# Kernel optimization log

Hardware: AMD Instinct MI355X
Metric: run time of the kernel (lower is better)

## Reference

```python
import jax, jax.numpy as jnp
import numpy as np

B, T, N, D, H = 16, 12, 325, 64, 4
E = 2600
NEG_SLOPE = 0.2
LN_EPS = 1e-5
SM_EPS = 1e-16


def setup_inputs() -> dict:
    key = jax.random.key(0)
    ks = jax.random.split(key, 8)
    x = jax.random.normal(ks[0], (B, T, N, D), dtype=jnp.float32)
    edge_index = jax.random.randint(ks[1], (2, E), 0, N, dtype=jnp.int64)
    W = jax.random.normal(ks[2], (D, H, D), dtype=jnp.float32) * 0.05   # lin weight, [in, heads, out]
    att_src = jax.random.normal(ks[3], (H, D), dtype=jnp.float32) * 0.05
    att_dst = jax.random.normal(ks[4], (H, D), dtype=jnp.float32) * 0.05
    bias = jnp.zeros((D,), dtype=jnp.float32)
    gamma = jnp.ones((D,), dtype=jnp.float32)
    beta = jnp.zeros((D,), dtype=jnp.float32)
    return {"x": x, "W": W, "att_src": att_src, "att_dst": att_dst,
            "bias": bias, "gamma": gamma, "beta": beta, "edge_index": edge_index}


def reference(x, W, att_src, att_dst, bias, gamma, beta, edge_index):
    b, t, n, d = x.shape
    bt = b * t
    xb = x.reshape(bt, n, d)

    # add self-loops (GATConv default add_self_loops=True)
    loops = jnp.arange(n, dtype=edge_index.dtype)
    src = jnp.concatenate([edge_index[0], loops])  # message source j
    dst = jnp.concatenate([edge_index[1], loops])  # message target i

    # per-head linear projection, node axis leading for segment ops: [N, BT, H, D]
    xp = jnp.einsum('bnd,dhf->nbhf', xb, W)

    a_src = jnp.einsum('nbhf,hf->nbh', xp, att_src)  # [N, BT, H]
    a_dst = jnp.einsum('nbhf,hf->nbh', xp, att_dst)

    alpha = a_src[src] + a_dst[dst]                  # [Etot, BT, H]
    alpha = jnp.where(alpha >= 0, alpha, NEG_SLOPE * alpha)

    # segment softmax over incoming edges of each dst node
    m = jax.ops.segment_max(alpha, dst, num_segments=n)        # [N, BT, H]
    e = jnp.exp(alpha - m[dst])
    s = jax.ops.segment_sum(e, dst, num_segments=n)            # [N, BT, H]
    coef = e / (s[dst] + SM_EPS)                               # [Etot, BT, H]

    # weighted scatter-sum aggregation
    msgs = coef[..., None] * xp[src]                           # [Etot, BT, H, D]
    out = jax.ops.segment_sum(msgs, dst, num_segments=n)       # [N, BT, H, D]

    out = out.mean(axis=2) + bias                              # concat=False -> head mean; [N, BT, D]
    out = out.transpose(1, 0, 2).reshape(b, t, n, d)

    # residual + LayerNorm
    y = x + out
    mu = y.mean(axis=-1, keepdims=True)
    var = y.var(axis=-1, keepdims=True)
    return (y - mu) * jax.lax.rsqrt(var + LN_EPS) * gamma + beta
```

## Files before the change

### kernel.cpp

```cpp
#include <hip/hip_runtime.h>

#define Nn 325
#define Dd 64
#define Hh 4
#define Ee 2600
#define BT 192
#define ETOT (Ee+Nn)
#define NROWS (BT*Nn)
#define MAXDEG 48

typedef __attribute__((ext_vector_type(8))) short bf16x8;
typedef __attribute__((ext_vector_type(4))) float f32x4;

static __device__ __forceinline__ short f2bf(float f) {
    union { float f; unsigned u; } v; v.f = f;
    unsigned r = v.u + 0x7fffu + ((v.u >> 16) & 1u);
    return (short)(r >> 16);
}
static __device__ __forceinline__ float bf_lo(unsigned p) {
    union { unsigned u; float f; } v; v.u = p << 16; return v.f;
}
static __device__ __forceinline__ float bf_hi(unsigned p) {
    union { unsigned u; float f; } v; v.u = p & 0xffff0000u; return v.f;
}

__global__ __launch_bounds__(256) void k_pre(
    const float* __restrict__ W, unsigned short* __restrict__ Wt,
    const int* __restrict__ ei, int* __restrict__ offs, int* __restrict__ elist)
{
    const int t = threadIdx.x;
    if (blockIdx.x < 64) {
        const int f = blockIdx.x * 256 + t;
        const int thr = f >> 6, idx = f & 63;
        const int tl = idx >> 4, kk = (idx >> 3) & 1, j = idx & 7;
        const int w = thr >> 6, lane = thr & 63;
        const int q = lane >> 4, l16 = lane & 15;
        Wt[f] = (unsigned short)f2bf(
            W[(size_t)(kk * 32 + q * 8 + j) * 256 + w * 64 + tl * 16 + l16]);
        return;
    }
    __shared__ int cnt[Nn + 1];
    __shared__ int cur[Nn];
    const int lane = t & 63;
    for (int i = t; i <= Nn; i += 256) cnt[i] = 0;
    __syncthreads();
    for (int e = t; e < ETOT; e += 256) {
        int d = (e < Ee) ? ei[Ee + e] : (e - Ee);
        atomicAdd(&cnt[d + 1], 1);
    }
    __syncthreads();
    if (t < 64) {
        int run = 0;
        for (int c = 0; c < 6; ++c) {
            int i = c * 64 + lane;
            int v = (i <= Nn) ? cnt[i] : 0;
            #pragma unroll
            for (int off = 1; off < 64; off <<= 1) {
                int u = __shfl_up(v, off);
                if (lane >= off) v += u;
            }
            v += run;
            if (i <= Nn) cnt[i] = v;
            run = __shfl(v, 63);
        }
    }
    __syncthreads();
    for (int i = t; i <= Nn; i += 256) offs[i] = cnt[i];
    for (int i = t; i < Nn; i += 256) cur[i] = cnt[i];
    __syncthreads();
    for (int e = t; e < ETOT; e += 256) {
        int s, d;
        if (e < Ee) { s = ei[e]; d = ei[Ee + e]; }
        else        { s = e - Ee; d = e - Ee; }
        int slot = atomicAdd(&cur[d], 1);
        elist[slot] = s;
    }
}

__global__ __launch_bounds__(256) void k_proj(
    const float* __restrict__ x, const unsigned short* __restrict__ Wt,
    const float* __restrict__ att_src, const float* __restrict__ att_dst,
    unsigned short* __restrict__ xp, float* __restrict__ asrc,
    float* __restrict__ adst)
{
    const int t = threadIdx.x;
    const int w = t >> 6;
    const int lane = t & 63;
    const int q = lane >> 4;
    const int l16 = lane & 15;
    const int g0 = blockIdx.x * 32;

    bf16x8 bfr[4][2];
    const bf16x8* wtp = (const bf16x8*)(Wt + (size_t)t * 64);
    #pragma unroll
    for (int tl = 0; tl < 4; ++tl)
        #pragma unroll
        for (int kk = 0; kk < 2; ++kk)
            bfr[tl][kk] = wtp[tl * 2 + kk];

    bf16x8 afr[2][2];
    #pragma unroll
    for (int rt = 0; rt < 2; ++rt)
        #pragma unroll
        for (int kk = 0; kk < 2; ++kk) {
            const float* xr = x + (size_t)(g0 + rt * 16 + l16) * Dd + kk * 32 + q * 8;
            float4 a0 = *(const float4*)xr;
            float4 a1 = *(const float4*)(xr + 4);
            afr[rt][kk][0]=f2bf(a0.x); afr[rt][kk][1]=f2bf(a0.y);
            afr[rt][kk][2]=f2bf(a0.z); afr[rt][kk][3]=f2bf(a0.w);
            afr[rt][kk][4]=f2bf(a1.x); afr[rt][kk][5]=f2bf(a1.y);
            afr[rt][kk][6]=f2bf(a1.z); afr[rt][kk][7]=f2bf(a1.w);
        }

    f32x4 acc[2][4];
    #pragma unroll
    for (int rt = 0; rt < 2; ++rt)
        #pragma unroll
        for (int tl = 0; tl < 4; ++tl) {
            acc[rt][tl] = (f32x4){0.f, 0.f, 0.f, 0.f};
            acc[rt][tl] = __builtin_amdgcn_mfma_f32_16x16x32_bf16(afr[rt][0], bfr[tl][0], acc[rt][tl], 0, 0, 0);
            acc[rt][tl] = __builtin_amdgcn_mfma_f32_16x16x32_bf16(afr[rt][1], bfr[tl][1], acc[rt][tl], 0, 0, 0);
        }

    float avs[4], avd[4];
    #pragma unroll
    for (int tl = 0; tl < 4; ++tl) {
        avs[tl] = att_src[w * 64 + tl * 16 + l16];
        avd[tl] = att_dst[w * 64 + tl * 16 + l16];
    }
    #pragma unroll
    for (int rt = 0; rt < 2; ++rt)
        #pragma unroll
        for (int r = 0; r < 4; ++r) {
            float ps = 0.f, pd = 0.f;
            #pragma unroll
            for (int tl = 0; tl < 4; ++tl) {
                ps = fmaf(acc[rt][tl][r], avs[tl], ps);
                pd = fmaf(acc[rt][tl][r], avd[tl], pd);
            }
            #pragma unroll
            for (int off = 1; off < 16; off <<= 1) {
                ps += __shfl_xor(ps, off);
                pd += __shfl_xor(pd, off);
            }
            if (l16 == 0) {
                asrc[(size_t)(g0 + rt * 16 + q * 4 + r) * Hh + w] = ps;
                adst[(size_t)(g0 + rt * 16 + q * 4 + r) * Hh + w] = pd;
            }
        }

    __shared__ unsigned short ldsXP[32][264];
    #pragma unroll
    for (int rt = 0; rt < 2; ++rt)
        #pragma unroll
        for (int tl = 0; tl < 4; ++tl)
            #pragma unroll
            for (int r = 0; r < 4; ++r)
                ldsXP[rt * 16 + q * 4 + r][(tl * 16 + l16) * 4 + w] =
                    (unsigned short)f2bf(acc[rt][tl][r]);
    __syncthreads();
    #pragma unroll
    for (int c = 0; c < 4; ++c) {
        int idx = c * 256 + t;
        int row = idx >> 5;
        int off = (idx & 31) * 8;
        uint4 v = *(const uint4*)&ldsXP[row][off];
        *(uint4*)(xp + (size_t)(g0 + row) * 256 + off) = v;
    }
}

__global__ __launch_bounds__(512) void k_aggr(
    const unsigned short* __restrict__ xp, const float* __restrict__ asrc,
    const float* __restrict__ adst, const int* __restrict__ offs,
    const int* __restrict__ elist, const float* __restrict__ x,
    const float* __restrict__ bias, const float* __restrict__ gamma,
    const float* __restrict__ beta, float* __restrict__ out)
{
    const int wv   = threadIdx.x >> 6;
    const int lane = threadIdx.x & 63;
    const int xcd  = blockIdx.x & 7;
    const int wid  = (blockIdx.x >> 3) * 8 + wv;
    if (wid >= 12 * Nn) return;
    const int btp  = wid / Nn;
    const int n    = wid - btp * Nn;
    const int half = lane >> 5;
    const int bt   = (xcd * 12 + btp) * 2 + half;
    const int btN  = bt * Nn;
    const int row_i = btN + n;
    const int o0 = offs[n];
    int deg = offs[n + 1] - o0;
    if (deg > MAXDEG) deg = MAXDEG;
    const int el = (lane >> 2) & 7;
    const int h  = lane & 3;

    __shared__ float coefS[8][2][MAXDEG][4];
    __shared__ int   jS[8][MAXDEG];

    const float adi = adst[(size_t)row_i * Hh + h];

    float areg[6];
    #pragma unroll
    for (int it = 0; it < 6; ++it) {
        const int e = it * 8 + el;
        float a = -3e38f;
        if (e < deg) {
            const int j = elist[o0 + e];
            if (half == 0 && h == 0) jS[wv][e] = j;
            a = asrc[(size_t)(btN + j) * Hh + h] + adi;
        }
        areg[it] = (a >= 0.f) ? a : 0.2f * a;
    }
    float m = areg[0];
    #pragma unroll
    for (int it = 1; it < 6; ++it) m = fmaxf(m, areg[it]);
    #pragma unroll
    for (int off = 4; off <= 16; off <<= 1) m = fmaxf(m, __shfl_xor(m, off));
    float s = 0.f;
    #pragma unroll
    for (int it = 0; it < 6; ++it) { areg[it] = __expf(areg[it] - m); s += areg[it]; }
    #pragma unroll
    for (int off = 4; off <= 16; off <<= 1) s += __shfl_xor(s, off);
    const float inv_s = 1.f / (s + 1e-16f);
    #pragma unroll
    for (int it = 0; it < 6; ++it) {
        const int e = it * 8 + el;
        if (e < deg) coefS[wv][half][e][h] = areg[it] * inv_s;
    }

    const int fl = lane & 31;
    const int f0 = fl * 2;
    const unsigned short* xpbt = xp + (size_t)btN * 256 + fl * 8;
    float a0=0,a1=0,a2=0,a3=0,a4=0,a5=0,a6=0,a7=0;
    int e2 = 0;
    for (; e2 + 2 <= deg; e2 += 2) {
        const int jb0 = jS[wv][e2];
        const int jb1 = jS[wv][e2 + 1];
        const float4 c0 = *(const float4*)coefS[wv][half][e2];
        const float4 c1 = *(const float4*)coefS[wv][half][e2 + 1];
        const uint4 r0 = *(const uint4*)(xpbt + (size_t)jb0 * 256);
        const uint4 r1 = *(const uint4*)(xpbt + (size_t)jb1 * 256);
        a0 = fmaf(c0.x, bf_lo(r0.x), a0); a1 = fmaf(c0.y, bf_hi(r0.x), a1);
        a2 = fmaf(c0.z, bf_lo(r0.y), a2); a3 = fmaf(c0.w, bf_hi(r0.y), a3);
        a4 = fmaf(c0.x, bf_lo(r0.z), a4); a5 = fmaf(c0.y, bf_hi(r0.z), a5);
        a6 = fmaf(c0.z, bf_lo(r0.w), a6); a7 = fmaf(c0.w, bf_hi(r0.w), a7);
        a0 = fmaf(c1.x, bf_lo(r1.x), a0); a1 = fmaf(c1.y, bf_hi(r1.x), a1);
        a2 = fmaf(c1.z, bf_lo(r1.y), a2); a3 = fmaf(c1.w, bf_hi(r1.y), a3);
        a4 = fmaf(c1.x, bf_lo(r1.z), a4); a5 = fmaf(c1.y, bf_hi(r1.z), a5);
        a6 = fmaf(c1.z, bf_lo(r1.w), a6); a7 = fmaf(c1.w, bf_hi(r1.w), a7);
    }
    if (e2 < deg) {
        const int jb0 = jS[wv][e2];
        const float4 c0 = *(const float4*)coefS[wv][half][e2];
        const uint4 r0 = *(const uint4*)(xpbt + (size_t)jb0 * 256);
        a0 = fmaf(c0.x, bf_lo(r0.x), a0); a1 = fmaf(c0.y, bf_hi(r0.x), a1);
        a2 = fmaf(c0.z, bf_lo(r0.y), a2); a3 = fmaf(c0.w, bf_hi(r0.y), a3);
        a4 = fmaf(c0.x, bf_lo(r0.z), a4); a5 = fmaf(c0.y, bf_hi(r0.z), a5);
        a6 = fmaf(c0.z, bf_lo(r0.w), a6); a7 = fmaf(c0.w, bf_hi(r0.w), a7);
    }

    float2 bi = *(const float2*)(bias + f0);
    float2 xv = *(const float2*)(x + (size_t)row_i * Dd + f0);
    float y0 = xv.x + (a0 + a1 + a2 + a3) * 0.25f + bi.x;
    float y1 = xv.y + (a4 + a5 + a6 + a7) * 0.25f + bi.y;
    float s1 = y0 + y1, s2v = y0 * y0 + y1 * y1;
    #pragma unroll
    for (int off = 1; off <= 16; off <<= 1) {
        s1  += __shfl_xor(s1, off);
        s2v += __shfl_xor(s2v, off);
    }
    float mu  = s1 * (1.f / Dd);
    float var = s2v * (1.f / Dd) - mu * mu;
    float r = rsqrtf(var + 1e-5f);
    float2 ga = *(const float2*)(gamma + f0);
    float2 be = *(const float2*)(beta + f0);
    float2 o;
    o.x = (y0 - mu) * r * ga.x + be.x;
    o.y = (y1 - mu) * r * ga.y + be.y;
    *(float2*)(out + (size_t)row_i * Dd + f0) = o;
}

extern "C" void kernel_launch(void* const* d_in, const int* in_sizes, int n_in,
                              void* d_out, int out_size, void* d_ws, size_t ws_size,
                              hipStream_t stream)
{
    const float* x       = (const float*)d_in[0];
    const float* W       = (const float*)d_in[1];
    const float* att_src = (const float*)d_in[2];
    const float* att_dst = (const float*)d_in[3];
    const float* bias    = (const float*)d_in[4];
    const float* gamma   = (const float*)d_in[5];
    const float* beta    = (const float*)d_in[6];
    const int*   ei      = (const int*)d_in[7];

    unsigned short* xp = (unsigned short*)d_ws;
    unsigned short* Wt = xp + (size_t)NROWS * 256;
    float* asrc  = (float*)(Wt + 16384);
    float* adst  = asrc + (size_t)NROWS * Hh;
    int*   offs  = (int*)(adst + (size_t)NROWS * Hh);
    int*   elist = offs + (Nn + 1);
    float* out   = (float*)d_out;

    hipLaunchKernelGGL(k_pre, dim3(65), dim3(256), 0, stream, W, Wt, ei, offs, elist);
    hipLaunchKernelGGL(k_proj, dim3(NROWS / 32), dim3(256), 0, stream,
                       x, Wt, att_src, att_dst, xp, asrc, adst);
    hipLaunchKernelGGL(k_aggr, dim3(8 * 488), dim3(512), 0, stream,
                       xp, asrc, adst, offs, elist, x, bias, gamma, beta, out);
}
```

Baseline: 138.7 us.

## Pre-convert x to bf16 in prep kernel, prescale edge indices, trim softmax loops

The prep kernel gets 488 extra blocks that convert x to bf16 into a workspace buffer, so the projection kernel loads bf16 fragments directly instead of converting fp32. Edge source indices are stored pre-multiplied by 16 so the aggregation kernel can use byte-offset addressing. The softmax loops now stop early based on node degree. The residual and LayerNorm parameter loads are hoisted ahead of the gather loop. The extra bf16 pass adds a full read and write of x, which may cost more than the conversion it removes from the projection kernel.

```diff
diff --git a/kernel.cpp b/kernel.cpp
--- a/kernel.cpp
+++ b/kernel.cpp
@@ -26,7 +26,8 @@
 
 __global__ __launch_bounds__(256) void k_pre(
     const float* __restrict__ W, unsigned short* __restrict__ Wt,
-    const int* __restrict__ ei, int* __restrict__ offs, int* __restrict__ elist)
+    const int* __restrict__ ei, int* __restrict__ offs, int* __restrict__ elist,
+    const float* __restrict__ x, unsigned short* __restrict__ xbf)
 {
     const int t = threadIdx.x;
     if (blockIdx.x < 64) {
@@ -39,6 +40,23 @@
             W[(size_t)(kk * 32 + q * 8 + j) * 256 + w * 64 + tl * 16 + l16]);
         return;
     }
+    if (blockIdx.x >= 65) {
+        const int bx = blockIdx.x - 65;
+        #pragma unroll
+        for (int k = 0; k < 8; ++k) {
+            const int idx = bx * 2048 + k * 256 + t;
+            if (idx < (NROWS * Dd) / 4) {
+                float4 v = ((const float4*)x)[idx];
+                ushort4 o;
+                o.x = (unsigned short)f2bf(v.x);
+                o.y = (unsigned short)f2bf(v.y);
+                o.z = (unsigned short)f2bf(v.z);
+                o.w = (unsigned short)f2bf(v.w);
+                ((ushort4*)xbf)[idx] = o;
+            }
+        }
+        return;
+    }
     __shared__ int cnt[Nn + 1];
     __shared__ int cur[Nn];
     const int lane = t & 63;
@@ -73,12 +91,12 @@
         if (e < Ee) { s = ei[e]; d = ei[Ee + e]; }
         else        { s = e - Ee; d = e - Ee; }
         int slot = atomicAdd(&cur[d], 1);
-        elist[slot] = s;
+        elist[slot] = s * 16;
     }
 }
 
 __global__ __launch_bounds__(256) void k_proj(
-    const float* __restrict__ x, const unsigned short* __restrict__ Wt,
+    const unsigned short* __restrict__ xbf, const unsigned short* __restrict__ Wt,
     const float* __restrict__ att_src, const float* __restrict__ att_dst,
     unsigned short* __restrict__ xp, float* __restrict__ asrc,
     float* __restrict__ adst)
@@ -102,15 +120,9 @@
     #pragma unroll
     for (int rt = 0; rt < 2; ++rt)
         #pragma unroll
-        for (int kk = 0; kk < 2; ++kk) {
-            const float* xr = x + (size_t)(g0 + rt * 16 + l16) * Dd + kk * 32 + q * 8;
-            float4 a0 = *(const float4*)xr;
-            float4 a1 = *(const float4*)(xr + 4);
-            afr[rt][kk][0]=f2bf(a0.x); afr[rt][kk][1]=f2bf(a0.y);
-            afr[rt][kk][2]=f2bf(a0.z); afr[rt][kk][3]=f2bf(a0.w);
-            afr[rt][kk][4]=f2bf(a1.x); afr[rt][kk][5]=f2bf(a1.y);
-            afr[rt][kk][6]=f2bf(a1.z); afr[rt][kk][7]=f2bf(a1.w);
-        }
+        for (int kk = 0; kk < 2; ++kk)
+            afr[rt][kk] = *(const bf16x8*)(
+                xbf + (size_t)(g0 + rt * 16 + l16) * Dd + kk * 32 + q * 8);
 
     f32x4 acc[2][4];
     #pragma unroll
@@ -186,50 +198,65 @@
     const int half = lane >> 5;
     const int bt   = (xcd * 12 + btp) * 2 + half;
     const int btN  = bt * Nn;
+    const int btN16 = btN * 16;
     const int row_i = btN + n;
     const int o0 = offs[n];
     int deg = offs[n + 1] - o0;
     if (deg > MAXDEG) deg = MAXDEG;
+    const int nit = (deg + 7) >> 3;
     const int el = (lane >> 2) & 7;
     const int h  = lane & 3;
+    const int h4 = h * 4;
 
     __shared__ float coefS[8][2][MAXDEG][4];
     __shared__ int   jS[8][MAXDEG];
 
     const float adi = adst[(size_t)row_i * Hh + h];
+    const char* asrc_c = (const char*)asrc;
 
     float areg[6];
+    float m = -3e38f;
     #pragma unroll
     for (int it = 0; it < 6; ++it) {
+        if (it >= nit) break;
         const int e = it * 8 + el;
         float a = -3e38f;
         if (e < deg) {
-            const int j = elist[o0 + e];
-            if (half == 0 && h == 0) jS[wv][e] = j;
-            a = asrc[(size_t)(btN + j) * Hh + h] + adi;
-        }
-        areg[it] = (a >= 0.f) ? a : 0.2f * a;
-    }
-    float m = areg[0];
-    #pragma unroll
-    for (int it = 1; it < 6; ++it) m = fmaxf(m, areg[it]);
+            const int j16 = elist[o0 + e];
+            if (half == 0 && h == 0) jS[wv][e] = j16;
+            a = *(const float*)(asrc_c + (size_t)(unsigned)(btN16 + j16) + h4) + adi;
+        }
+        a = (a >= 0.f) ? a : 0.2f * a;
+        areg[it] = a;
+        m = fmaxf(m, a);
+    }
     #pragma unroll
     for (int off = 4; off <= 16; off <<= 1) m = fmaxf(m, __shfl_xor(m, off));
     float s = 0.f;
     #pragma unroll
-    for (int it = 0; it < 6; ++it) { areg[it] = __expf(areg[it] - m); s += areg[it]; }
+    for (int it = 0; it < 6; ++it) {
+        if (it >= nit) break;
+        areg[it] = __expf(areg[it] - m);
+        s += areg[it];
+    }
     #pragma unroll
     for (int off = 4; off <= 16; off <<= 1) s += __shfl_xor(s, off);
     const float inv_s = 1.f / (s + 1e-16f);
     #pragma unroll
     for (int it = 0; it < 6; ++it) {
+        if (it >= nit) break;
         const int e = it * 8 + el;
         if (e < deg) coefS[wv][half][e][h] = areg[it] * inv_s;
     }
 
     const int fl = lane & 31;
     const int f0 = fl * 2;
-    const unsigned short* xpbt = xp + (size_t)btN * 256 + fl * 8;
+    const float2 bi = *(const float2*)(bias + f0);
+    const float2 xv = *(const float2*)(x + (size_t)row_i * Dd + f0);
+    const float2 ga = *(const float2*)(gamma + f0);
+    const float2 be = *(const float2*)(beta + f0);
+
+    const char* xpb = (const char*)xp + (size_t)btN16 * 32 + fl * 16;
     float a0=0,a1=0,a2=0,a3=0,a4=0,a5=0,a6=0,a7=0;
     int e2 = 0;
     for (; e2 + 2 <= deg; e2 += 2) {
@@ -237,8 +264,8 @@
         const int jb1 = jS[wv][e2 + 1];
         const float4 c0 = *(const float4*)coefS[wv][half][e2];
         const float4 c1 = *(const float4*)coefS[wv][half][e2 + 1];
-        const uint4 r0 = *(const uint4*)(xpbt + (size_t)jb0 * 256);
-        const uint4 r1 = *(const uint4*)(xpbt + (size_t)jb1 * 256);
+        const uint4 r0 = *(const uint4*)(xpb + (size_t)(unsigned)jb0 * 32);
+        const uint4 r1 = *(const uint4*)(xpb + (size_t)(unsigned)jb1 * 32);
         a0 = fmaf(c0.x, bf_lo(r0.x), a0); a1 = fmaf(c0.y, bf_hi(r0.x), a1);
         a2 = fmaf(c0.z, bf_lo(r0.y), a2); a3 = fmaf(c0.w, bf_hi(r0.y), a3);
         a4 = fmaf(c0.x, bf_lo(r0.z), a4); a5 = fmaf(c0.y, bf_hi(r0.z), a5);
@@ -251,15 +278,13 @@
     if (e2 < deg) {
         const int jb0 = jS[wv][e2];
         const float4 c0 = *(const float4*)coefS[wv][half][e2];
-        const uint4 r0 = *(const uint4*)(xpbt + (size_t)jb0 * 256);
+        const uint4 r0 = *(const uint4*)(xpb + (size_t)(unsigned)jb0 * 32);
         a0 = fmaf(c0.x, bf_lo(r0.x), a0); a1 = fmaf(c0.y, bf_hi(r0.x), a1);
         a2 = fmaf(c0.z, bf_lo(r0.y), a2); a3 = fmaf(c0.w, bf_hi(r0.y), a3);
         a4 = fmaf(c0.x, bf_lo(r0.z), a4); a5 = fmaf(c0.y, bf_hi(r0.z), a5);
         a6 = fmaf(c0.z, bf_lo(r0.w), a6); a7 = fmaf(c0.w, bf_hi(r0.w), a7);
     }
 
-    float2 bi = *(const float2*)(bias + f0);
-    float2 xv = *(const float2*)(x + (size_t)row_i * Dd + f0);
     float y0 = xv.x + (a0 + a1 + a2 + a3) * 0.25f + bi.x;
     float y1 = xv.y + (a4 + a5 + a6 + a7) * 0.25f + bi.y;
     float s1 = y0 + y1, s2v = y0 * y0 + y1 * y1;
@@ -271,8 +296,6 @@
     float mu  = s1 * (1.f / Dd);
     float var = s2v * (1.f / Dd) - mu * mu;
     float r = rsqrtf(var + 1e-5f);
-    float2 ga = *(const float2*)(gamma + f0);
-    float2 be = *(const float2*)(beta + f0);
     float2 o;
     o.x = (y0 - mu) * r * ga.x + be.x;
     o.y = (y1 - mu) * r * ga.y + be.y;
@@ -292,17 +315,19 @@
     const float* beta    = (const float*)d_in[6];
     const int*   ei      = (const int*)d_in[7];
 
-    unsigned short* xp = (unsigned short*)d_ws;
-    unsigned short* Wt = xp + (size_t)NROWS * 256;
-    float* asrc  = (float*)(Wt + 16384);
+    unsigned short* xp  = (unsigned short*)d_ws;
+    unsigned short* Wt  = xp + (size_t)NROWS * 256;
+    unsigned short* xbf = Wt + 16384;
+    float* asrc  = (float*)(xbf + (size_t)NROWS * Dd);
     float* adst  = asrc + (size_t)NROWS * Hh;
     int*   offs  = (int*)(adst + (size_t)NROWS * Hh);
     int*   elist = offs + (Nn + 1);
     float* out   = (float*)d_out;
 
-    hipLaunchKernelGGL(k_pre, dim3(65), dim3(256), 0, stream, W, Wt, ei, offs, elist);
+    hipLaunchKernelGGL(k_pre, dim3(65 + 488), dim3(256), 0, stream,
+                       W, Wt, ei, offs, elist, x, xbf);
     hipLaunchKernelGGL(k_proj, dim3(NROWS / 32), dim3(256), 0, stream,
-                       x, Wt, att_src, att_dst, xp, asrc, adst);
+                       xbf, Wt, att_src, att_dst, xp, asrc, adst);
     hipLaunchKernelGGL(k_aggr, dim3(8 * 488), dim3(512), 0, stream,
                        xp, asrc, adst, offs, elist, x, bias, gamma, beta, out);
 }
```

Measured after the change: 137.2 us. About the same (-1.1%).
